# Kernel tuning notes

Measured on AMD Instinct MI355X. Metric: run time of the kernel, lower is better.

## Reference

```python
import jax, jax.numpy as jnp
import numpy as np
import math

DIM = 1024
SEQ = 2048
BATCH = 4
LN_EPS = 1e-5


def _linear_params(key, fan_in, fan_out):
    # torch nn.Linear default init: U(-1/sqrt(fan_in), 1/sqrt(fan_in))
    k1, k2 = jax.random.split(key)
    bound = 1.0 / math.sqrt(fan_in)
    W = jax.random.uniform(k1, (fan_out, fan_in), minval=-bound, maxval=bound, dtype=jnp.float32)
    b = jax.random.uniform(k2, (fan_out,), minval=-bound, maxval=bound, dtype=jnp.float32)
    return W, b


def setup_inputs() -> dict:
    key = jax.random.key(0)
    ks = jax.random.split(key, 9)
    x = jax.random.normal(ks[0], (BATCH, SEQ, DIM), dtype=jnp.float32)
    base_phases = jax.random.normal(ks[1], (SEQ, DIM), dtype=jnp.float32) * math.pi
    Wk, bk = _linear_params(ks[2], DIM, DIM)
    Wv, bv = _linear_params(ks[3], DIM, DIM)
    Wq, bq = _linear_params(ks[4], DIM, DIM)
    Wkm, bkm = _linear_params(ks[5], DIM, DIM)
    Wqm, bqm = _linear_params(ks[6], DIM, DIM)
    Wo, bo = _linear_params(ks[7], DIM, DIM)
    mod_scale = jnp.ones((1,), dtype=jnp.float32) * 0.1
    ln_g = jnp.ones((DIM,), dtype=jnp.float32)
    ln_b = jnp.zeros((DIM,), dtype=jnp.float32)
    return dict(x=x, base_phases=base_phases, Wk=Wk, bk=bk, Wv=Wv, bv=bv,
                Wq=Wq, bq=bq, Wkm=Wkm, bkm=bkm, Wqm=Wqm, bqm=bqm,
                mod_scale=mod_scale, ln_g=ln_g, ln_b=ln_b, Wo=Wo, bo=bo)


def _lin(x, W, b):
    return jnp.einsum('bsd,ed->bse', x, W) + b


def reference(x, base_phases, Wk, bk, Wv, bv, Wq, bq, Wkm, bkm, Wqm, bqm,
              mod_scale, ln_g, ln_b, Wo, bo):
    dim = x.shape[-1]
    base_phase = base_phases[None, :, :]  # [1, S, D]
    key = _lin(x, Wk, bk)
    value = _lin(x, Wv, bv)
    query = _lin(x, Wq, bq)
    key_phase = base_phase + _lin(key, Wkm, bkm) * mod_scale
    query_phase = base_phase + _lin(query, Wqm, bqm) * mod_scale
    # bind value with complex phasor exp(i*key_phase), prefix-sum over seq
    mem_real = jnp.cumsum(value * jnp.cos(key_phase), axis=1)
    mem_imag = jnp.cumsum(value * jnp.sin(key_phase), axis=1)
    # phase-matched retrieval: Re(mem * exp(-i*query_phase))
    retrieved = (mem_real * jnp.cos(query_phase) + mem_imag * jnp.sin(query_phase))
    retrieved = retrieved / math.sqrt(dim)
    # LayerNorm then output projection
    mu = jnp.mean(retrieved, axis=-1, keepdims=True)
    var = jnp.var(retrieved, axis=-1, keepdims=True)
    normed = (retrieved - mu) * jax.lax.rsqrt(var + LN_EPS) * ln_g + ln_b
    out = _lin(normed, Wo, bo)
    return x + out
```

## Files before the change

### kernel.cpp

```cpp
#include <hip/hip_runtime.h>
#include <math.h>

#define DIM 1024
#define SEQ 2048
#define BATCH 4
#define ROWS (BATCH*SEQ)
#define CHUNKS 128
#define CLEN (SEQ/CHUNKS)
#define N3 3072
#define LN_EPS 1e-5f
#define NTK 16

typedef unsigned short ushort_t;
typedef __attribute__((ext_vector_type(8))) short bf16x8;
typedef __attribute__((ext_vector_type(4))) float f32x4;

static const size_t NE = (size_t)ROWS * DIM;
static const size_t WN = (size_t)DIM * DIM;

__device__ inline ushort_t f2bf(float f) {
    union { float f; unsigned u; } v; v.f = f;
    unsigned r = v.u + 0x7FFFu + ((v.u >> 16) & 1u);
    return (ushort_t)(r >> 16);
}
__device__ inline float bf2f(ushort_t u) { return __uint_as_float((unsigned)u << 16); }
__device__ inline float bf_lo(unsigned p) { return __uint_as_float(p << 16); }
__device__ inline float bf_hi(unsigned p) { return __uint_as_float(p & 0xFFFF0000u); }
__device__ inline float bfq(float f) { return bf2f(f2bf(f)); }

__global__ __launch_bounds__(256)
void conv_all_k(const float* __restrict__ x,  const float* __restrict__ Wv,
                const float* __restrict__ Wo, const float* __restrict__ Wkm,
                const float* __restrict__ Wqm,
                ushort_t* __restrict__ xbf,   ushort_t* __restrict__ W3,
                ushort_t* __restrict__ wo_b,  ushort_t* __restrict__ wkm_b,
                ushort_t* __restrict__ wqm_b)
{
    size_t e = ((size_t)blockIdx.x * 256 + threadIdx.x) * 8;
    const float* src; ushort_t* dst; size_t off;
    if      (e < NE)          { src = x;   dst = xbf;   off = e; }
    else if (e < NE + WN)     { src = Wv;  dst = W3;    off = e - NE; }
    else if (e < NE + 2*WN)   { src = Wo;  dst = wo_b;  off = e - NE - 2*WN + WN; }
    else if (e < NE + 3*WN)   { src = Wkm; dst = wkm_b; off = e - NE - 2*WN; }
    else                      { src = Wqm; dst = wqm_b; off = e - NE - 3*WN; }
    float4 a = *(const float4*)(src + off);
    float4 b = *(const float4*)(src + off + 4);
    ushort4 lo, hi;
    lo.x = f2bf(a.x); lo.y = f2bf(a.y); lo.z = f2bf(a.z); lo.w = f2bf(a.w);
    hi.x = f2bf(b.x); hi.y = f2bf(b.y); hi.z = f2bf(b.z); hi.w = f2bf(b.w);
    *(ushort4*)(dst + off) = lo;
    *(ushort4*)(dst + off + 4) = hi;
}

__global__ __launch_bounds__(256)
void transpose2_k(const float* __restrict__ Wk, const float* __restrict__ Wq,
                  ushort_t* __restrict__ wkT, ushort_t* __restrict__ wqT)
{
    const float* in = blockIdx.z ? Wq : Wk;
    ushort_t* out   = blockIdx.z ? wqT : wkT;
    __shared__ ushort_t tile[32][33];
    const int bx = blockIdx.x, by = blockIdx.y;
    const int tx = threadIdx.x & 31, ty = threadIdx.x >> 5;
    #pragma unroll
    for (int j = 0; j < 4; ++j) {
        int r = by * 32 + ty + j * 8;
        tile[ty + j * 8][tx] = f2bf(in[(size_t)r * DIM + bx * 32 + tx]);
    }
    __syncthreads();
    #pragma unroll
    for (int j = 0; j < 4; ++j) {
        int r = bx * 32 + ty + j * 8;
        out[(size_t)r * DIM + by * 32 + tx] = tile[tx][ty + j * 8];
    }
}

__global__ __launch_bounds__(256)
void matvec2_k(const float* __restrict__ Wkm, const float* __restrict__ bk,
               const float* __restrict__ bkm, float* __restrict__ bck,
               const float* __restrict__ Wqm, const float* __restrict__ bq,
               const float* __restrict__ bqm, float* __restrict__ bcq)
{
    int z = blockIdx.y;
    const float* Wm  = z ? Wqm : Wkm;
    const float* bi  = z ? bq  : bk;
    const float* bo_ = z ? bqm : bkm;
    float* bc        = z ? bcq : bck;
    int e = blockIdx.x * 4 + (threadIdx.x >> 6);
    int l = threadIdx.x & 63;
    float s = 0.f;
    #pragma unroll
    for (int j = 0; j < DIM / 64; ++j)
        s += Wm[(size_t)e * DIM + l + j * 64] * bi[l + j * 64];
    #pragma unroll
    for (int o = 32; o >= 1; o >>= 1) s += __shfl_down(s, o);
    if (l == 0) bc[e] = s + bo_[e];
}

__global__ __launch_bounds__(256)
void gemm_combine2(const ushort_t* __restrict__ A0, const ushort_t* __restrict__ W0,
                   ushort_t* __restrict__ C0,
                   const ushort_t* __restrict__ A1, const ushort_t* __restrict__ W1,
                   ushort_t* __restrict__ C1)
{
    const ushort_t* A = blockIdx.z ? A1 : A0;
    const ushort_t* W = blockIdx.z ? W1 : W0;
    ushort_t*       C = blockIdx.z ? C1 : C0;
    __shared__ ushort_t As[128 * 32];
    __shared__ ushort_t Bs[128 * 32];
    const int bm = blockIdx.x * 128;
    const int bn = blockIdx.y * 128;
    const int t = threadIdx.x;
    const int lane = t & 63;
    const int w = t >> 6, wr = w >> 1, wc = w & 1;
    f32x4 acc[4][4] = {};
    const int fr = lane & 15;
    const int kc = (lane >> 4) * 8;
    for (int k0 = 0; k0 < DIM; k0 += 32) {
        #pragma unroll
        for (int i = 0; i < 2; ++i) {
            int c = t + i * 256;
            int row = c >> 2;
            int col = (c & 3) * 8;
            const ushort_t* ga = A + (size_t)(bm + row) * DIM + k0 + col;
            __builtin_amdgcn_global_load_lds(
                (const __attribute__((address_space(1))) void*)ga,
                (__attribute__((address_space(3))) void*)(As + (size_t)c * 8), 16, 0, 0);
            const ushort_t* gb = W + (size_t)(bn + row) * DIM + k0 + col;
            __builtin_amdgcn_global_load_lds(
                (const __attribute__((address_space(1))) void*)gb,
                (__attribute__((address_space(3))) void*)(Bs + (size_t)c * 8), 16, 0, 0);
        }
        __syncthreads();
        bf16x8 af[4], bw[4];
        #pragma unroll
        for (int m2 = 0; m2 < 4; ++m2)
            af[m2] = *(const bf16x8*)(As + (wr * 64 + m2 * 16 + fr) * 32 + kc);
        #pragma unroll
        for (int n2 = 0; n2 < 4; ++n2)
            bw[n2] = *(const bf16x8*)(Bs + (wc * 64 + n2 * 16 + fr) * 32 + kc);
        #pragma unroll
        for (int m2 = 0; m2 < 4; ++m2)
            #pragma unroll
            for (int n2 = 0; n2 < 4; ++n2)
                acc[m2][n2] = __builtin_amdgcn_mfma_f32_16x16x32_bf16(
                    af[m2], bw[n2], acc[m2][n2], 0, 0, 0);
        __syncthreads();
    }
    const int fc = lane & 15;
    const int r0 = (lane >> 4) * 4;
    #pragma unroll
    for (int m2 = 0; m2 < 4; ++m2)
        #pragma unroll
        for (int n2 = 0; n2 < 4; ++n2) {
            int col = bn + wc * 64 + n2 * 16 + fc;
            #pragma unroll
            for (int r = 0; r < 4; ++r) {
                int row = bm + wr * 64 + m2 * 16 + r0 + r;
                C[(size_t)row * DIM + col] = f2bf(acc[m2][n2][r]);
            }
        }
}

template<int MODE, int BN>
__global__ __launch_bounds__(512)
void gemm_pipe(const ushort_t* __restrict__ A, const ushort_t* __restrict__ W,
               const float* __restrict__ bias, const float* __restrict__ resid,
               void* __restrict__ Cout, int N)
{
    constexpr int NF   = BN / 64;
    constexpr int BUFU = 16384 + BN * 64;
    __shared__ __align__(16) ushort_t lds[2 * BUFU];

    const int bm = blockIdx.x * 256;
    const int bn = blockIdx.y * BN;
    const int t = threadIdx.x;
    const int lane = t & 63;
    const int w = t >> 6;
    const int wr = w >> 2;
    const int wc = w & 3;
    const int fr = lane & 15;
    const int hi = lane >> 4;

    f32x4 acc[8][NF] = {};

    auto SA = [&](int kt, ushort_t* buf, int h) {
        #pragma unroll
        for (int i = 0; i < 2; ++i) {
            int c = t + i * 512;
            int row = c >> 2, sl = c & 3, sg = sl ^ ((row >> 1) & 3);
            const ushort_t* g = A + (size_t)(bm + row) * 1024 + kt * 64 + h * 32 + sg * 8;
            __builtin_amdgcn_global_load_lds(
                (const __attribute__((address_space(1))) void*)g,
                (__attribute__((address_space(3))) void*)(buf + h * 8192 + (size_t)c * 8),
                16, 0, 0);
        }
    };
    auto SB = [&](int kt, ushort_t* buf, int h) {
        #pragma unroll
        for (int i = 0; i < BN / 128; ++i) {
            int c = t + i * 512;
            int row = c >> 2, sl = c & 3, sg = sl ^ ((row >> 1) & 3);
            const ushort_t* g = W + (size_t)(bn + row) * 1024 + kt * 64 + h * 32 + sg * 8;
            __builtin_amdgcn_global_load_lds(
                (const __attribute__((address_space(1))) void*)g,
                (__attribute__((address_space(3))) void*)(buf + 16384 + h * (BN * 32) + (size_t)c * 8),
                16, 0, 0);
        }
    };

#define GPHASE(KK, MH, STAGE_STMT)                                           \
    {                                                                        \
        bf16x8 af[4];                                                        \
        _Pragma("unroll")                                                    \
        for (int j = 0; j < 4; ++j) {                                        \
            int row = wr * 128 + ((MH) * 4 + j) * 16 + fr;                   \
            af[j] = *(const bf16x8*)(As + (KK) * 8192 + row * 32 +           \
                                     (hi ^ ((row >> 1) & 3)) * 8);           \
        }                                                                    \
        if ((MH) == 0) {                                                     \
            _Pragma("unroll")                                                \
            for (int nf = 0; nf < NF; ++nf) {                                \
                int row = wc * (BN / 4) + nf * 16 + fr;                      \
                bw[nf] = *(const bf16x8*)(Bs + (KK) * (BN * 32) + row * 32 + \
                                          (hi ^ ((row >> 1) & 3)) * 8);      \
            }                                                                \
        }                                                                    \
        STAGE_STMT;                                                          \
        __builtin_amdgcn_s_barrier();                                        \
        asm volatile("s_waitcnt lgkmcnt(0)" ::: "memory");                   \
        __builtin_amdgcn_sched_barrier(0);                                   \
        __builtin_amdgcn_s_setprio(1);                                       \
        _Pragma("unroll")                                                    \
        for (int j = 0; j < 4; ++j)                                          \
            _Pragma("unroll")                                                \
            for (int nf = 0; nf < NF; ++nf)                                  \
                acc[(MH) * 4 + j][nf] = __builtin_amdgcn_mfma_f32_16x16x32_bf16( \
                    af[j], bw[nf], acc[(MH) * 4 + j][nf], 0, 0, 0);          \
        __builtin_amdgcn_s_setprio(0);                                       \
        __builtin_amdgcn_s_barrier();                                        \
    }

    SA(0, lds, 0); SB(0, lds, 0); SA(0, lds, 1); SB(0, lds, 1);

    for (int tt = 0; tt < NTK; ++tt) {
        ushort_t* base = lds + (tt & 1) * BUFU;
        ushort_t* nbuf = lds + ((tt + 1) & 1) * BUFU;
        const ushort_t* As = base;
        const ushort_t* Bs = base + 16384;
        const bool st = (tt + 1 < NTK);
        bf16x8 bw[NF];

        if constexpr (NF == 4) asm volatile("s_waitcnt vmcnt(4)" ::: "memory");
        else                   asm volatile("s_waitcnt vmcnt(3)" ::: "memory");
        __builtin_amdgcn_s_barrier();

        GPHASE(0, 0, if (st) SA(tt + 1, nbuf, 0));
        GPHASE(0, 1, if (st) SB(tt + 1, nbuf, 0));

        if (st) {
            if constexpr (NF == 4) asm volatile("s_waitcnt vmcnt(4)" ::: "memory");
            else                   asm volatile("s_waitcnt vmcnt(3)" ::: "memory");
        } else {
            asm volatile("s_waitcnt vmcnt(0)" ::: "memory");
        }
        __builtin_amdgcn_s_barrier();

        GPHASE(1, 0, if (st) SA(tt + 1, nbuf, 1));
        GPHASE(1, 1, if (st) SB(tt + 1, nbuf, 1));
    }
#undef GPHASE

    const int fc = fr;
    const int r0 = hi * 4;
    #pragma unroll
    for (int m2 = 0; m2 < 8; ++m2)
        #pragma unroll
        for (int n2 = 0; n2 < NF; ++n2) {
            int col = bn + wc * (BN / 4) + n2 * 16 + fc;
            float bv;
            if (MODE == 6) bv = (col < 1024) ? bias[col] : 0.0f;
            else           bv = bias[col];
            #pragma unroll
            for (int r = 0; r < 4; ++r) {
                int row = bm + wr * 128 + m2 * 16 + r0 + r;
                size_t idx = (size_t)row * N + col;
                float v = acc[m2][n2][r] + bv;
                if (MODE == 4) ((float*)Cout)[idx] = v + resid[idx];
                else           ((ushort_t*)Cout)[idx] = f2bf(v);
            }
        }
}

__global__ __launch_bounds__(256)
void phase_scan1_k(const ushort_t* __restrict__ act3, const float* __restrict__ bp,
                   const float* __restrict__ bck, const float* __restrict__ ms_p,
                   unsigned* __restrict__ ab,
                   float* __restrict__ sumr, float* __restrict__ sumi)
{
    const int blk = blockIdx.x;
    const int b = blk >> 7;
    const int c = blk & (CHUNKS - 1);
    const int d0 = threadIdx.x * 4;
    const float ms = ms_p[0];
    const float4 bc4 = *(const float4*)(bck + d0);
    float sr0 = 0.f, sr1 = 0.f, sr2 = 0.f, sr3 = 0.f;
    float si0 = 0.f, si1 = 0.f, si2 = 0.f, si3 = 0.f;
    const size_t row0 = (size_t)b * SEQ + (size_t)c * CLEN;

    #pragma unroll 2
    for (int s = 0; s < CLEN; ++s) {
        size_t row = row0 + s;
        ushort4 v4 = *(const ushort4*)(act3 + row * N3 + d0);
        ushort4 k4 = *(const ushort4*)(act3 + row * N3 + 1024 + d0);
        float4 bp4 = *(const float4*)(bp + ((size_t)(c * CLEN + s)) * DIM + d0);
        uint4 o;
        float vv, kp, sn, cs, ar, ai;
        vv = bf2f(v4.x); kp = bp4.x + (bf2f(k4.x) + bc4.x) * ms;
        sincosf(kp, &sn, &cs); ar = bfq(vv * cs); ai = bfq(vv * sn);
        sr0 += ar; si0 += ai;
        o.x = (unsigned)f2bf(ar) | ((unsigned)f2bf(ai) << 16);
        vv = bf2f(v4.y); kp = bp4.y + (bf2f(k4.y) + bc4.y) * ms;
        sincosf(kp, &sn, &cs); ar = bfq(vv * cs); ai = bfq(vv * sn);
        sr1 += ar; si1 += ai;
        o.y = (unsigned)f2bf(ar) | ((unsigned)f2bf(ai) << 16);
        vv = bf2f(v4.z); kp = bp4.z + (bf2f(k4.z) + bc4.z) * ms;
        sincosf(kp, &sn, &cs); ar = bfq(vv * cs); ai = bfq(vv * sn);
        sr2 += ar; si2 += ai;
        o.z = (unsigned)f2bf(ar) | ((unsigned)f2bf(ai) << 16);
        vv = bf2f(v4.w); kp = bp4.w + (bf2f(k4.w) + bc4.w) * ms;
        sincosf(kp, &sn, &cs); ar = bfq(vv * cs); ai = bfq(vv * sn);
        sr3 += ar; si3 += ai;
        o.w = (unsigned)f2bf(ar) | ((unsigned)f2bf(ai) << 16);
        *(uint4*)(ab + row * DIM + d0) = o;
    }
    int sgid = (b * CHUNKS + c) * DIM + d0;
    *(float4*)(sumr + sgid) = make_float4(sr0, sr1, sr2, sr3);
    *(float4*)(sumi + sgid) = make_float4(si0, si1, si2, si3);
}

__global__ __launch_bounds__(256)
void scan_pass2(float* __restrict__ sumr, float* __restrict__ sumi)
{
    int wid  = (blockIdx.x * 256 + threadIdx.x) >> 6;
    int lane = threadIdx.x & 63;
    int b = wid >> 10;
    int d = wid & (DIM - 1);
    int i0 = (b * CHUNKS + 2 * lane) * DIM + d;
    int i1 = i0 + DIM;
    float r0 = sumr[i0], r1 = sumr[i1];
    float s0 = sumi[i0], s1 = sumi[i1];
    float pr = r0 + r1, pi = s0 + s1;
    float er = pr, ei = pi;
    #pragma unroll
    for (int o = 1; o < 64; o <<= 1) {
        float tr = __shfl_up(er, o);
        float ti = __shfl_up(ei, o);
        if (lane >= o) { er += tr; ei += ti; }
    }
    er -= pr; ei -= pi;
    sumr[i0] = er;       sumi[i0] = ei;
    sumr[i1] = er + r0;  sumi[i1] = ei + s0;
}

__global__ __launch_bounds__(256)
void scan3_ln_k(const unsigned* __restrict__ ab, const ushort_t* __restrict__ act3,
                const float* __restrict__ bp, const float* __restrict__ bcq,
                const float* __restrict__ ms_p,
                const float* __restrict__ sumr, const float* __restrict__ sumi,
                const float* __restrict__ g, const float* __restrict__ beta,
                ushort_t* __restrict__ normbf)
{
    const int blk = blockIdx.x;
    const int b = blk >> 7;
    const int c = blk & (CHUNKS - 1);
    const int t = threadIdx.x;
    const int d0 = t * 4;
    const float ms = ms_p[0];
    const float4 bq4 = *(const float4*)(bcq + d0);
    const float4 gv  = *(const float4*)(g + d0);
    const float4 btv = *(const float4*)(beta + d0);
    const float inv_sqrt_dim = 0.03125f;

    int sgid = (b * CHUNKS + c) * DIM + d0;
    float4 rrv = *(const float4*)(sumr + sgid);
    float4 riv = *(const float4*)(sumi + sgid);
    float rr0 = rrv.x, rr1 = rrv.y, rr2 = rrv.z, rr3 = rrv.w;
    float ri0 = riv.x, ri1 = riv.y, ri2 = riv.z, ri3 = riv.w;

    const size_t row0 = (size_t)b * SEQ + (size_t)c * CLEN;
    __shared__ float red[16];
    const int wv = t >> 6, lane = t & 63;

    uint4   abv = *(const uint4*)(ab + row0 * DIM + d0);
    ushort4 q4  = *(const ushort4*)(act3 + row0 * N3 + 2048 + d0);
    float4  bp4 = *(const float4*)(bp + (size_t)(c * CLEN) * DIM + d0);

    for (int s = 0; s < CLEN; ++s) {
        uint4 abc = abv; ushort4 qc = q4; float4 bpc = bp4;
        if (s + 1 < CLEN) {
            size_t row = row0 + s + 1;
            abv = *(const uint4*)(ab + row * DIM + d0);
            q4  = *(const ushort4*)(act3 + row * N3 + 2048 + d0);
            bp4 = *(const float4*)(bp + (size_t)(c * CLEN + s + 1) * DIM + d0);
        }
        float r0g, r1g, r2g, r3g, qp, sq, cq;
        rr0 += bf_lo(abc.x); ri0 += bf_hi(abc.x);
        qp = bpc.x + (bf2f(qc.x) + bq4.x) * ms; sincosf(qp, &sq, &cq);
        r0g = (rr0 * cq + ri0 * sq) * inv_sqrt_dim;
        rr1 += bf_lo(abc.y); ri1 += bf_hi(abc.y);
        qp = bpc.y + (bf2f(qc.y) + bq4.y) * ms; sincosf(qp, &sq, &cq);
        r1g = (rr1 * cq + ri1 * sq) * inv_sqrt_dim;
        rr2 += bf_lo(abc.z); ri2 += bf_hi(abc.z);
        qp = bpc.z + (bf2f(qc.z) + bq4.z) * ms; sincosf(qp, &sq, &cq);
        r2g = (rr2 * cq + ri2 * sq) * inv_sqrt_dim;
        rr3 += bf_lo(abc.w); ri3 += bf_hi(abc.w);
        qp = bpc.w + (bf2f(qc.w) + bq4.w) * ms; sincosf(qp, &sq, &cq);
        r3g = (rr3 * cq + ri3 * sq) * inv_sqrt_dim;

        float ssum = r0g + r1g + r2g + r3g;
        float ssq  = r0g*r0g + r1g*r1g + r2g*r2g + r3g*r3g;
        #pragma unroll
        for (int o = 32; o >= 1; o >>= 1) {
            ssum += __shfl_down(ssum, o);
            ssq  += __shfl_down(ssq, o);
        }
        float* rd = red + (s & 1) * 8;
        if (lane == 0) { rd[wv] = ssum; rd[wv + 4] = ssq; }
        __syncthreads();
        if (t == 0) {
            rd[0] = rd[0] + rd[1] + rd[2] + rd[3];
            rd[4] = rd[4] + rd[5] + rd[6] + rd[7];
        }
        __syncthreads();
        float mu  = rd[0] * (1.0f / DIM);
        float var = rd[4] * (1.0f / DIM) - mu * mu;
        float rstd = rsqrtf(var + LN_EPS);
        ushort4 o;
        o.x = f2bf((r0g - mu) * rstd * gv.x + btv.x);
        o.y = f2bf((r1g - mu) * rstd * gv.y + btv.y);
        o.z = f2bf((r2g - mu) * rstd * gv.z + btv.z);
        o.w = f2bf((r3g - mu) * rstd * gv.w + btv.w);
        *(ushort4*)(normbf + (row0 + s) * DIM + d0) = o;
    }
}

extern "C" void kernel_launch(void* const* d_in, const int* in_sizes, int n_in,
                              void* d_out, int out_size, void* d_ws, size_t ws_size,
                              hipStream_t stream)
{
    const float* x   = (const float*)d_in[0];
    const float* bp  = (const float*)d_in[1];
    const float* Wk  = (const float*)d_in[2];
    const float* bk  = (const float*)d_in[3];
    const float* Wv  = (const float*)d_in[4];
    const float* bv  = (const float*)d_in[5];
    const float* Wq  = (const float*)d_in[6];
    const float* bq  = (const float*)d_in[7];
    const float* Wkm = (const float*)d_in[8];
    const float* bkm = (const float*)d_in[9];
    const float* Wqm = (const float*)d_in[10];
    const float* bqm = (const float*)d_in[11];
    const float* ms  = (const float*)d_in[12];
    const float* lng = (const float*)d_in[13];
    const float* lnb = (const float*)d_in[14];
    const float* Wo  = (const float*)d_in[15];
    const float* bo  = (const float*)d_in[16];
    float* out = (float*)d_out;

    unsigned* ab     = (unsigned*)d_ws;
    ushort_t* act3   = (ushort_t*)(ab + NE);
    ushort_t* xbf    = act3 + (size_t)ROWS * N3;
    ushort_t* normbf = xbf + NE;
    ushort_t* W3     = normbf + NE;
    ushort_t* wo_b   = W3 + (size_t)N3 * DIM;
    ushort_t* wkm_b  = wo_b + WN;
    ushort_t* wqm_b  = wkm_b + WN;
    ushort_t* wkT_b  = wqm_b + WN;
    ushort_t* wqT_b  = wkT_b + WN;
    float* bck       = (float*)(wqT_b + WN);
    float* bcq       = bck + DIM;
    float* sumr      = bcq + DIM;
    float* sumi      = sumr + (size_t)BATCH * CHUNKS * DIM;

    conv_all_k<<<(int)((NE + 4 * WN) / 2048), 256, 0, stream>>>(
        x, Wv, Wo, Wkm, Wqm, xbf, W3, wo_b, wkm_b, wqm_b);
    dim3 tg(32, 32, 2);
    transpose2_k<<<tg, 256, 0, stream>>>(Wk, Wq, wkT_b, wqT_b);
    dim3 mg(DIM / 4, 2);
    matvec2_k<<<mg, 256, 0, stream>>>(Wkm, bk, bkm, bck, Wqm, bq, bqm, bcq);
    dim3 gw(DIM / 128, DIM / 128, 2);
    gemm_combine2<<<gw, 256, 0, stream>>>(wkm_b, wkT_b, W3 + WN,
                                          wqm_b, wqT_b, W3 + 2 * WN);

    dim3 g3(32, N3 / 256);
    gemm_pipe<6, 256><<<g3, 512, 0, stream>>>(xbf, W3, bv, nullptr, act3, N3);

    phase_scan1_k<<<BATCH * CHUNKS, 256, 0, stream>>>(act3, bp, bck, ms,
                                                      ab, sumr, sumi);
    scan_pass2<<<(BATCH * DIM) / 4, 256, 0, stream>>>(sumr, sumi);
    scan3_ln_k<<<BATCH * CHUNKS, 256, 0, stream>>>(ab, act3, bp, bcq, ms,
                                                   sumr, sumi, lng, lnb, normbf);

    dim3 gg(32, DIM / 128);
    gemm_pipe<4, 128><<<gg, 512, 0, stream>>>(normbf, wo_b, bo, x, out, DIM);
}
```

Before: 193.2 us.

## Switch QKV GEMM to 192-wide N tiles with full-K B staging

New measurement: 185.0 us. 1.04x faster.

```diff
diff --git a/kernel.cpp b/kernel.cpp
--- a/kernel.cpp
+++ b/kernel.cpp
@@ -195,17 +195,26 @@
                 16, 0, 0);
         }
     };
-    auto SB = [&](int kt, ushort_t* buf, int h) {
-        #pragma unroll
-        for (int i = 0; i < BN / 128; ++i) {
+    auto SBfull = [&](int kt, ushort_t* buf) {
+        #pragma unroll
+        for (int i = 0; i < 3; ++i) {
             int c = t + i * 512;
-            int row = c >> 2, sl = c & 3, sg = sl ^ ((row >> 1) & 3);
-            const ushort_t* g = W + (size_t)(bn + row) * 1024 + kt * 64 + h * 32 + sg * 8;
+            int row = c >> 3, sl = c & 7, sg = sl ^ (row & 7);
+            const ushort_t* g = W + (size_t)(bn + row) * 1024 + kt * 64 + sg * 8;
             __builtin_amdgcn_global_load_lds(
                 (const __attribute__((address_space(1))) void*)g,
-                (__attribute__((address_space(3))) void*)(buf + 16384 + h * (BN * 32) + (size_t)c * 8),
+                (__attribute__((address_space(3))) void*)(buf + 16384 + (size_t)c * 8),
                 16, 0, 0);
         }
+    };
+    auto SBh = [&](int kt, ushort_t* buf, int h) {
+        int c = t;
+        int row = c >> 2, sl = c & 3, sg = sl ^ ((row >> 1) & 3);
+        const ushort_t* g = W + (size_t)(bn + row) * 1024 + kt * 64 + h * 32 + sg * 8;
+        __builtin_amdgcn_global_load_lds(
+            (const __attribute__((address_space(1))) void*)g,
+            (__attribute__((address_space(3))) void*)(buf + 16384 + h * (BN * 32) + (size_t)c * 8),
+            16, 0, 0);
     };
 
 #define GPHASE(KK, MH, STAGE_STMT)                                           \
@@ -215,14 +224,18 @@
         for (int j = 0; j < 4; ++j) {                                        \
             int row = wr * 128 + ((MH) * 4 + j) * 16 + fr;                   \
             af[j] = *(const bf16x8*)(As + (KK) * 8192 + row * 32 +           \
-                                     (hi ^ ((row >> 1) & 3)) * 8);           \
+                                     ((hi ^ ((row >> 1) & 3))) * 8);         \
         }                                                                    \
         if ((MH) == 0) {                                                     \
             _Pragma("unroll")                                                \
             for (int nf = 0; nf < NF; ++nf) {                                \
                 int row = wc * (BN / 4) + nf * 16 + fr;                      \
-                bw[nf] = *(const bf16x8*)(Bs + (KK) * (BN * 32) + row * 32 + \
-                                          (hi ^ ((row >> 1) & 3)) * 8);      \
+                if (BN == 192)                                               \
+                    bw[nf] = *(const bf16x8*)(Bs + row * 64 +                \
+                                 (((KK) * 4 + hi) ^ (row & 7)) * 8);         \
+                else                                                         \
+                    bw[nf] = *(const bf16x8*)(Bs + (KK) * (BN * 32) + row * 32 + \
+                                 ((hi ^ ((row >> 1) & 3))) * 8);             \
             }                                                                \
         }                                                                    \
         STAGE_STMT;                                                          \
@@ -240,7 +253,11 @@
         __builtin_amdgcn_s_barrier();                                        \
     }
 
-    SA(0, lds, 0); SB(0, lds, 0); SA(0, lds, 1); SB(0, lds, 1);
+    if constexpr (BN == 192) {
+        SBfull(0, lds); SA(0, lds, 0); SA(0, lds, 1);
+    } else {
+        SA(0, lds, 0); SBh(0, lds, 0); SA(0, lds, 1); SBh(0, lds, 1);
+    }
 
     for (int tt = 0; tt < NTK; ++tt) {
         ushort_t* base = lds + (tt & 1) * BUFU;
@@ -250,23 +267,33 @@
         const bool st = (tt + 1 < NTK);
         bf16x8 bw[NF];
 
-        if constexpr (NF == 4) asm volatile("s_waitcnt vmcnt(4)" ::: "memory");
-        else                   asm volatile("s_waitcnt vmcnt(3)" ::: "memory");
+        if constexpr (BN == 192) asm volatile("s_waitcnt vmcnt(2)" ::: "memory");
+        else                     asm volatile("s_waitcnt vmcnt(3)" ::: "memory");
         __builtin_amdgcn_s_barrier();
 
-        GPHASE(0, 0, if (st) SA(tt + 1, nbuf, 0));
-        GPHASE(0, 1, if (st) SB(tt + 1, nbuf, 0));
+        if constexpr (BN == 192) {
+            GPHASE(0, 0, if (st) SBfull(tt + 1, nbuf));
+            GPHASE(0, 1, if (st) SA(tt + 1, nbuf, 0));
+        } else {
+            GPHASE(0, 0, if (st) SA(tt + 1, nbuf, 0));
+            GPHASE(0, 1, if (st) SBh(tt + 1, nbuf, 0));
+        }
 
         if (st) {
-            if constexpr (NF == 4) asm volatile("s_waitcnt vmcnt(4)" ::: "memory");
-            else                   asm volatile("s_waitcnt vmcnt(3)" ::: "memory");
+            if constexpr (BN == 192) asm volatile("s_waitcnt vmcnt(5)" ::: "memory");
+            else                     asm volatile("s_waitcnt vmcnt(3)" ::: "memory");
         } else {
             asm volatile("s_waitcnt vmcnt(0)" ::: "memory");
         }
         __builtin_amdgcn_s_barrier();
 
-        GPHASE(1, 0, if (st) SA(tt + 1, nbuf, 1));
-        GPHASE(1, 1, if (st) SB(tt + 1, nbuf, 1));
+        if constexpr (BN == 192) {
+            GPHASE(1, 0, if (st) SA(tt + 1, nbuf, 1));
+            GPHASE(1, 1, );
+        } else {
+            GPHASE(1, 0, if (st) SA(tt + 1, nbuf, 1));
+            GPHASE(1, 1, if (st) SBh(tt + 1, nbuf, 1));
+        }
     }
 #undef GPHASE
 
@@ -492,8 +519,8 @@
     gemm_combine2<<<gw, 256, 0, stream>>>(wkm_b, wkT_b, W3 + WN,
                                           wqm_b, wqT_b, W3 + 2 * WN);
 
-    dim3 g3(32, N3 / 256);
-    gemm_pipe<6, 256><<<g3, 512, 0, stream>>>(xbf, W3, bv, nullptr, act3, N3);
+    dim3 g3(32, N3 / 192);
+    gemm_pipe<6, 192><<<g3, 512, 0, stream>>>(xbf, W3, bv, nullptr, act3, N3);
 
     phase_scan1_k<<<BATCH * CHUNKS, 256, 0, stream>>>(act3, bp, bck, ms,
                                                       ab, sumr, sumi);
```
